# Kernel tuning notes

Measured on AMD Instinct MI355X. Metric: run time of the kernel, lower is better.

Reference implementation:

```python
import jax, jax.numpy as jnp
import numpy as np

EMA_BETA = 0.9
NUM_HEADS = 16

def causal_prefix_ema(x, beta):
    # x: [b, t, d]; s_t = beta*s_{t-1} + (1-beta)*x_t, s_{-1}=0
    def step(s, xt):
        s = beta * s + (1.0 - beta) * xt
        return s, s
    s0 = jnp.zeros_like(x[:, 0, :])
    _, ys = jax.lax.scan(step, s0, jnp.swapaxes(x, 0, 1))  # [t, b, d]
    return jnp.swapaxes(ys, 0, 1)

def setup_inputs() -> dict:
    key = jax.random.key(0)
    ks = jax.random.split(key, 9)
    b, t, d = 2, 1024, 2048
    sc = lambda fan_in: 1.0 / np.sqrt(fan_in)
    return {
        "x": jax.random.normal(ks[0], (b, t, d), jnp.float32),
        "l3_memory": jax.random.normal(ks[1], (b, 1, d), jnp.float32),
        "wq": jax.random.normal(ks[2], (d, d), jnp.float32) * sc(d),
        "wk": jax.random.normal(ks[3], (d, d), jnp.float32) * sc(d),
        "wv": jax.random.normal(ks[4], (d, d), jnp.float32) * sc(d),
        "wo": jax.random.normal(ks[5], (d, d), jnp.float32) * sc(d),
        "rw1": jax.random.normal(ks[6], (d // 2, d), jnp.float32) * sc(d),
        "rb1": jnp.zeros((d // 2,), jnp.float32),
        "rw2": jax.random.normal(ks[7], (3, d // 2), jnp.float32) * sc(d // 2),
        "rb2": jnp.zeros((3,), jnp.float32),
    }

def reference(x, l3_memory, wq, wk, wv, wo, rw1, rb1, rw2, rb2):
    b, t, d = x.shape
    h = NUM_HEADS
    dh = d // h
    scale = 1.0 / np.sqrt(dh)

    q = x @ wq.T                                   # [b,t,d]
    l1 = x
    l2 = causal_prefix_ema(x, EMA_BETA)            # [b,t,d]
    l3 = jnp.broadcast_to(l3_memory, (b, t, d))    # repeat retrieval memory to length t

    # router: MLP(Q) -> softmax over 3 levels
    hdn = jax.nn.silu(q @ rw1.T + rb1)
    lam = jax.nn.softmax(hdn @ rw2.T + rb2, axis=-1)  # [b,t,3]

    fused = lam[..., 0:1] * l1 + lam[..., 1:2] * l2 + lam[..., 2:3] * l3

    def heads(y):
        return jnp.swapaxes(y.reshape(b, t, h, dh), 1, 2)  # [b,h,t,dh]

    qh = heads(q)
    kh = heads(fused @ wk.T)
    vh = heads(fused @ wv.T)

    scores = jnp.einsum("bhqd,bhkd->bhqk", qh, kh) * scale
    causal = jnp.tril(jnp.ones((t, t), bool))
    scores = jnp.where(causal, scores, jnp.finfo(scores.dtype).min)
    attn = jax.nn.softmax(scores, axis=-1)
    out = jnp.einsum("bhqk,bhkd->bhqd", attn, vh)

    out = jnp.swapaxes(out, 1, 2).reshape(b, t, d) @ wo.T
    return (out, kh, vh, lam)
```

## Files before the change

kernel.cpp:

```cpp
#include <hip/hip_runtime.h>
#include <hip/hip_bf16.h>
#include <math.h>

#define B_  2
#define T_  1024
#define D_  2048
#define H_  16
#define DH_ 128
#define M_  2048
#define DR_ 1024
#define CH_  16
#define NCH_ 64

typedef __attribute__((ext_vector_type(8))) short short8;
typedef __attribute__((ext_vector_type(4))) short sh4;
typedef __attribute__((ext_vector_type(4))) float f32x4;

__device__ __forceinline__ void gld16(const __hip_bfloat16* g, __hip_bfloat16* l) {
  __builtin_amdgcn_global_load_lds(
      (const __attribute__((address_space(1))) unsigned int*)g,
      (__attribute__((address_space(3))) unsigned int*)l, 16, 0, 0);
}

template<int BM, int CMODE, bool SILU>
__global__ __launch_bounds__(256)
void gemm_mfma(const __hip_bfloat16* __restrict__ A,
               const __hip_bfloat16* __restrict__ Bm,
               const float* __restrict__ bias,
               float* __restrict__ C, __hip_bfloat16* __restrict__ Cb,
               float* __restrict__ C2, __hip_bfloat16* __restrict__ Cb2,
               int M, int N, int K)
{
  constexpr int NI = BM / 32;
  constexpr int AC = BM / 64;
  __shared__ __hip_bfloat16 As[2][2][BM * 32];
  __shared__ __hip_bfloat16 Bs[2][2][128 * 32];
  const int tid  = threadIdx.x;
  const int wave = tid >> 6;
  const int lane = tid & 63;
  const int m0 = blockIdx.y * BM;
  const int n0 = blockIdx.x * 128;
  const int wm = (wave >> 1) * (BM / 2);
  const int wn = (wave & 1) * 64;

  const int srow = lane >> 2;
  const int scol = (lane & 3) * 8;
  const __hip_bfloat16* Ag = A  + (size_t)(m0 + wave * (BM / 4) + srow) * K + scol;
  const __hip_bfloat16* Bg = Bm + (size_t)(n0 + wave * 32 + srow) * K + scol;

  const int fr = lane & 15;
  const int fk = (lane >> 4) * 8;

  f32x4 acc[NI][4];
  #pragma unroll
  for (int i = 0; i < NI; ++i)
    #pragma unroll
    for (int j = 0; j < 4; ++j) acc[i][j] = (f32x4)0.f;

  auto stage = [&](int bf, int k0) {
    #pragma unroll
    for (int h = 0; h < 2; ++h) {
      #pragma unroll
      for (int c = 0; c < AC; ++c)
        gld16(Ag + k0 + h * 32 + (size_t)(c * 16) * K,
              &As[bf][h][(wave * (BM / 4) + c * 16) * 32]);
      #pragma unroll
      for (int c = 0; c < 2; ++c)
        gld16(Bg + k0 + h * 32 + (size_t)(c * 16) * K,
              &Bs[bf][h][(wave * 32 + c * 16) * 32]);
    }
  };

  stage(0, 0);
  __syncthreads();
  int cur = 0;
  for (int k0 = 0; k0 < K; k0 += 64) {
    if (k0 + 64 < K) stage(cur ^ 1, k0 + 64);
    #pragma unroll
    for (int h = 0; h < 2; ++h) {
      short8 af[NI], bfr[4];
      #pragma unroll
      for (int i = 0; i < NI; ++i)
        af[i]  = *(const short8*)&As[cur][h][(wm + i * 16 + fr) * 32 + fk];
      #pragma unroll
      for (int j = 0; j < 4; ++j)
        bfr[j] = *(const short8*)&Bs[cur][h][(wn + j * 16 + fr) * 32 + fk];
      #pragma unroll
      for (int i = 0; i < NI; ++i)
        #pragma unroll
        for (int j = 0; j < 4; ++j)
          acc[i][j] = __builtin_amdgcn_mfma_f32_16x16x32_bf16(af[i], bfr[j], acc[i][j], 0, 0, 0);
    }
    __syncthreads();
    cur ^= 1;
  }

  #pragma unroll
  for (int i = 0; i < NI; ++i) {
    #pragma unroll
    for (int j = 0; j < 4; ++j) {
      const int row0 = m0 + wm + i * 16 + (lane >> 4) * 4;
      const int col  = n0 + wn + j * 16 + (lane & 15);
      float vr[4];
      #pragma unroll
      for (int r = 0; r < 4; ++r) {
        float v = acc[i][j][r];
        if (bias) v += bias[col];
        if (SILU) v = v / (1.f + __expf(-v));
        vr[r] = v;
      }
      if (CMODE == 0) {
        #pragma unroll
        for (int r = 0; r < 4; ++r) C[(size_t)(row0 + r) * N + col] = vr[r];
      } else if (CMODE == 1) {
        #pragma unroll
        for (int r = 0; r < 4; ++r) Cb[(size_t)(row0 + r) * N + col] = __float2bfloat16(vr[r]);
      } else {
        const int bb = row0 >> 10, t0v = row0 & 1023;
        if (col < D_) {
          const int hh = col >> 7, dd = col & 127;
          #pragma unroll
          for (int r = 0; r < 4; ++r) {
            const size_t idx = (((size_t)(bb * H_ + hh)) * T_ + t0v + r) * DH_ + dd;
            C[idx] = vr[r];
            Cb[idx] = __float2bfloat16(vr[r]);
          }
        } else {
          const int c2 = col - D_;
          const int hh = c2 >> 7, dd = c2 & 127;
          #pragma unroll
          for (int r = 0; r < 4; ++r)
            C2[(((size_t)(bb * H_ + hh)) * T_ + t0v + r) * DH_ + dd] = vr[r];
          __hip_bfloat16 tmp[4];
          #pragma unroll
          for (int r = 0; r < 4; ++r) tmp[r] = __float2bfloat16(vr[r]);
          *(sh4*)(Cb2 + (((size_t)(bb * H_ + hh)) * DH_ + dd) * T_ + t0v) = *(const sh4*)tmp;
        }
      }
    }
  }
}

__global__ __launch_bounds__(256)
void prep_scan(const float* __restrict__ x, __hip_bfloat16* __restrict__ xb,
               float* __restrict__ l2)
{
  const int b  = blockIdx.z;
  const int t0 = blockIdx.y * CH_;
  const int d  = blockIdx.x * 1024 + threadIdx.x * 4;
  const float* xp = x  + (size_t)b * T_ * D_ + d;
  float*       lp = l2 + (size_t)b * T_ * D_ + d;
  __hip_bfloat16* xo = xb + (size_t)b * T_ * D_ + d;
  float4 s = make_float4(0.f, 0.f, 0.f, 0.f);
  #pragma unroll 4
  for (int t = t0; t < t0 + CH_; ++t) {
    float4 v = *(const float4*)(xp + (size_t)t * D_);
    __hip_bfloat16 tmp[4] = {__float2bfloat16(v.x), __float2bfloat16(v.y),
                             __float2bfloat16(v.z), __float2bfloat16(v.w)};
    *(sh4*)(xo + (size_t)t * D_) = *(const sh4*)tmp;
    s.x = 0.9f * s.x + 0.1f * v.x;
    s.y = 0.9f * s.y + 0.1f * v.y;
    s.z = 0.9f * s.z + 0.1f * v.z;
    s.w = 0.9f * s.w + 0.1f * v.w;
    *(float4*)(lp + (size_t)t * D_) = s;
  }
}

__global__ __launch_bounds__(256)
void cvt5(const float* __restrict__ s0, const float* __restrict__ s1,
          const float* __restrict__ s2, const float* __restrict__ s3,
          const float* __restrict__ s4,
          __hip_bfloat16* d0, __hip_bfloat16* d1, __hip_bfloat16* d2,
          __hip_bfloat16* d3, __hip_bfloat16* d4,
          int n0, int n1, int n2, int n3, int n4)
{
  const float* s; __hip_bfloat16* d; int n;
  switch (blockIdx.y) {
    case 0: s = s0; d = d0; n = n0; break;
    case 1: s = s1; d = d1; n = n1; break;
    case 2: s = s2; d = d2; n = n2; break;
    case 3: s = s3; d = d3; n = n3; break;
    default: s = s4; d = d4; n = n4; break;
  }
  const int i = (blockIdx.x * 256 + threadIdx.x) * 8;
  if (i < n) {
    float4 a = *(const float4*)(s + i);
    float4 b = *(const float4*)(s + i + 4);
    __hip_bfloat16 t[8] = {__float2bfloat16(a.x), __float2bfloat16(a.y),
                           __float2bfloat16(a.z), __float2bfloat16(a.w),
                           __float2bfloat16(b.x), __float2bfloat16(b.y),
                           __float2bfloat16(b.z), __float2bfloat16(b.w)};
    *(short8*)(d + i) = *(const short8*)t;
  }
}

__global__ __launch_bounds__(64)
void ema_carry(const float* __restrict__ l2loc, float* __restrict__ carry)
{
  const int i = blockIdx.x * 64 + threadIdx.x;
  const int b = i >> 11, d = i & 2047;
  const float A = 0.18530201888518416f;
  float c = 0.f;
  carry[((size_t)b * NCH_ + 0) * D_ + d] = 0.f;
  for (int ch = 1; ch < NCH_; ++ch) {
    const float lf = l2loc[((size_t)b * T_ + ch * CH_ - 1) * D_ + d];
    c = lf + A * c;
    carry[((size_t)b * NCH_ + ch) * D_ + d] = c;
  }
}

__global__ __launch_bounds__(256)
void router_kernel(const float* __restrict__ hdn, const float* __restrict__ rw2,
                   const float* __restrict__ rb2, float* __restrict__ lam)
{
  const int lane = threadIdx.x & 63;
  const int w    = threadIdx.x >> 6;
  const int m    = blockIdx.x * 4 + w;
  const float* hp = hdn + (size_t)m * DR_;
  float s0 = 0.f, s1 = 0.f, s2 = 0.f;
  for (int k = lane * 4; k < DR_; k += 256) {
    float4 h4 = *(const float4*)(hp + k);
    float4 w0 = *(const float4*)(rw2 + k);
    float4 w1 = *(const float4*)(rw2 + DR_ + k);
    float4 w2 = *(const float4*)(rw2 + 2 * DR_ + k);
    s0 += h4.x * w0.x + h4.y * w0.y + h4.z * w0.z + h4.w * w0.w;
    s1 += h4.x * w1.x + h4.y * w1.y + h4.z * w1.z + h4.w * w1.w;
    s2 += h4.x * w2.x + h4.y * w2.y + h4.z * w2.z + h4.w * w2.w;
  }
  #pragma unroll
  for (int off = 32; off > 0; off >>= 1) {
    s0 += __shfl_down(s0, off);
    s1 += __shfl_down(s1, off);
    s2 += __shfl_down(s2, off);
  }
  if (lane == 0) {
    s0 += rb2[0]; s1 += rb2[1]; s2 += rb2[2];
    float mx = fmaxf(s0, fmaxf(s1, s2));
    float e0 = __expf(s0 - mx), e1 = __expf(s1 - mx), e2 = __expf(s2 - mx);
    float inv = 1.f / (e0 + e1 + e2);
    lam[(size_t)m * 3 + 0] = e0 * inv;
    lam[(size_t)m * 3 + 1] = e1 * inv;
    lam[(size_t)m * 3 + 2] = e2 * inv;
  }
}

__global__ __launch_bounds__(256)
void fuse_bf16(const float* __restrict__ x, const float* __restrict__ l2,
               const float* __restrict__ l3m, const float* __restrict__ lam,
               const float* __restrict__ carry, __hip_bfloat16* __restrict__ fb)
{
  const int i8 = blockIdx.x * 256 + threadIdx.x;
  const int m  = i8 >> 8;
  const int c  = (i8 & 255) << 3;
  const int b  = m >> 10;
  const int t  = m & 1023;
  const int ch = t >> 4, off = t & 15;
  const float p = __expf((float)(off + 1) * -0.105360515657f);
  const float w0 = lam[m * 3 + 0], w1 = lam[m * 3 + 1], w2 = lam[m * 3 + 2];
  const float* xp = x   + (size_t)m * D_ + c;
  const float* ep = l2  + (size_t)m * D_ + c;
  const float* gp = l3m + (size_t)b * D_ + c;
  const float* cp = carry + ((size_t)b * NCH_ + ch) * D_ + c;
  __hip_bfloat16 tmp[8];
  #pragma unroll
  for (int q = 0; q < 2; ++q) {
    float4 xv = *(const float4*)(xp + q * 4);
    float4 ev = *(const float4*)(ep + q * 4);
    float4 gv = *(const float4*)(gp + q * 4);
    float4 cv = *(const float4*)(cp + q * 4);
    tmp[q * 4 + 0] = __float2bfloat16(w0 * xv.x + w1 * (ev.x + p * cv.x) + w2 * gv.x);
    tmp[q * 4 + 1] = __float2bfloat16(w0 * xv.y + w1 * (ev.y + p * cv.y) + w2 * gv.y);
    tmp[q * 4 + 2] = __float2bfloat16(w0 * xv.z + w1 * (ev.z + p * cv.z) + w2 * gv.z);
    tmp[q * 4 + 3] = __float2bfloat16(w0 * xv.w + w1 * (ev.w + p * cv.w) + w2 * gv.w);
  }
  *(short8*)(fb + (size_t)m * D_ + c) = *(const short8*)tmp;
}

__global__ __launch_bounds__(256)
void flash_mfma(const __hip_bfloat16* __restrict__ qg,
                const __hip_bfloat16* __restrict__ kg,
                const __hip_bfloat16* __restrict__ vg,
                __hip_bfloat16* __restrict__ og)
{
  __shared__ __hip_bfloat16 Ks[64 * 136];
  __shared__ __hip_bfloat16 Vt[128 * 72];
  __shared__ __hip_bfloat16 Ps[64 * 72];
  const int tid  = threadIdx.x;
  const int wave = tid >> 6, lane = tid & 63;
  const int L    = blockIdx.x;
  const int halfg = L >> 8, idx = L & 255;
  const int bh = (idx >> 4) | (halfg << 4);
  const int qt = halfg ? (15 - (idx & 15)) : (idx & 15);
  const int b = bh >> 4, h = bh & 15;
  const int q0 = qt * 64;
  const int lo = lane & 15, hi = lane >> 4;

  short8 aq[4];
  {
    const __hip_bfloat16* qsrc = qg + (size_t)(b * T_ + q0 + wave * 16 + lo) * D_ + h * DH_;
    #pragma unroll
    for (int kk = 0; kk < 4; ++kk)
      aq[kk] = *(const short8*)(qsrc + kk * 32 + hi * 8);
  }

  f32x4 oacc[8];
  #pragma unroll
  for (int i = 0; i < 8; ++i) oacc[i] = (f32x4)0.f;
  float mrow[4] = {-INFINITY, -INFINITY, -INFINITY, -INFINITY};
  float lrow[4] = {0.f, 0.f, 0.f, 0.f};

  const __hip_bfloat16* kbp = kg + (size_t)bh * T_ * DH_;
  const __hip_bfloat16* vbp = vg + (size_t)bh * DH_ * T_;
  const float scale = 0.08838834764831845f;

  short8 kreg[4], vreg[4];
  auto load_tile = [&](int k0) {
    #pragma unroll
    for (int i = 0; i < 4; ++i) {
      const int ci = tid + 256 * i;
      const int r = ci >> 4, j = ci & 15;
      kreg[i] = *(const short8*)(kbp + (size_t)(k0 + r) * DH_ + j * 8);
      const int dd = ci >> 3, j2 = ci & 7;
      vreg[i] = *(const short8*)(vbp + (size_t)dd * T_ + k0 + j2 * 8);
    }
  };

  load_tile(0);
  for (int kt = 0; kt <= qt; ++kt) {
    #pragma unroll
    for (int i = 0; i < 4; ++i) {
      const int ci = tid + 256 * i;
      const int r = ci >> 4, j = ci & 15;
      *(short8*)&Ks[r * 136 + j * 8] = kreg[i];
      const int dd = ci >> 3, j2 = ci & 7;
      *(short8*)&Vt[dd * 72 + j2 * 8] = vreg[i];
    }
    __syncthreads();
    if (kt < qt) load_tile((kt + 1) * 64);

    f32x4 sc[4];
    __builtin_amdgcn_s_setprio(1);
    #pragma unroll
    for (int nt = 0; nt < 4; ++nt) {
      sc[nt] = (f32x4)0.f;
      #pragma unroll
      for (int kk = 0; kk < 4; ++kk) {
        short8 bk = *(const short8*)&Ks[(nt * 16 + lo) * 136 + kk * 32 + hi * 8];
        sc[nt] = __builtin_amdgcn_mfma_f32_16x16x32_bf16(aq[kk], bk, sc[nt], 0, 0, 0);
      }
    }
    __builtin_amdgcn_s_setprio(0);
    #pragma unroll
    for (int nt = 0; nt < 4; ++nt)
      #pragma unroll
      for (int r = 0; r < 4; ++r) sc[nt][r] *= scale;
    if (kt == qt) {
      const int qrow = q0 + wave * 16 + hi * 4;
      #pragma unroll
      for (int nt = 0; nt < 4; ++nt) {
        const int key = qt * 64 + nt * 16 + lo;
        #pragma unroll
        for (int r = 0; r < 4; ++r)
          if (key > qrow + r) sc[nt][r] = -1e30f;
      }
    }
    float alpha[4];
    #pragma unroll
    for (int r = 0; r < 4; ++r) {
      float mx = fmaxf(fmaxf(sc[0][r], sc[1][r]), fmaxf(sc[2][r], sc[3][r]));
      mx = fmaxf(mx, __shfl_xor(mx, 1));
      mx = fmaxf(mx, __shfl_xor(mx, 2));
      mx = fmaxf(mx, __shfl_xor(mx, 4));
      mx = fmaxf(mx, __shfl_xor(mx, 8));
      const float nm = fmaxf(mrow[r], mx);
      alpha[r] = __expf(mrow[r] - nm);
      mrow[r] = nm;
      float ls = 0.f;
      #pragma unroll
      for (int nt = 0; nt < 4; ++nt) {
        float p = __expf(sc[nt][r] - nm);
        sc[nt][r] = p;
        ls += p;
      }
      ls += __shfl_xor(ls, 1);
      ls += __shfl_xor(ls, 2);
      ls += __shfl_xor(ls, 4);
      ls += __shfl_xor(ls, 8);
      lrow[r] = lrow[r] * alpha[r] + ls;
    }
    #pragma unroll
    for (int nt = 0; nt < 4; ++nt)
      #pragma unroll
      for (int r = 0; r < 4; ++r)
        Ps[(wave * 16 + hi * 4 + r) * 72 + nt * 16 + lo] = __float2bfloat16(sc[nt][r]);
    #pragma unroll
    for (int n2 = 0; n2 < 8; ++n2)
      #pragma unroll
      for (int r = 0; r < 4; ++r) oacc[n2][r] *= alpha[r];
    short8 ap[2];
    #pragma unroll
    for (int k2 = 0; k2 < 2; ++k2)
      ap[k2] = *(const short8*)&Ps[(wave * 16 + lo) * 72 + k2 * 32 + hi * 8];
    __builtin_amdgcn_s_setprio(1);
    #pragma unroll
    for (int n2 = 0; n2 < 8; ++n2) {
      #pragma unroll
      for (int k2 = 0; k2 < 2; ++k2) {
        short8 bv = *(const short8*)&Vt[(n2 * 16 + lo) * 72 + k2 * 32 + hi * 8];
        oacc[n2] = __builtin_amdgcn_mfma_f32_16x16x32_bf16(ap[k2], bv, oacc[n2], 0, 0, 0);
      }
    }
    __builtin_amdgcn_s_setprio(0);
    __syncthreads();
  }

  float inv[4];
  #pragma unroll
  for (int r = 0; r < 4; ++r) inv[r] = 1.f / lrow[r];
  __hip_bfloat16* od = og + (size_t)(b * T_ + q0 + wave * 16 + hi * 4) * D_ + h * DH_;
  #pragma unroll
  for (int n2 = 0; n2 < 8; ++n2)
    #pragma unroll
    for (int r = 0; r < 4; ++r)
      od[(size_t)r * D_ + n2 * 16 + lo] = __float2bfloat16(oacc[n2][r] * inv[r]);
}

extern "C" void kernel_launch(void* const* d_in, const int* in_sizes, int n_in,
                              void* d_out, int out_size, void* d_ws, size_t ws_size,
                              hipStream_t stream)
{
  const float* x   = (const float*)d_in[0];
  const float* l3m = (const float*)d_in[1];
  const float* wq  = (const float*)d_in[2];
  const float* wk  = (const float*)d_in[3];
  const float* wv  = (const float*)d_in[4];
  const float* wo  = (const float*)d_in[5];
  const float* rw1 = (const float*)d_in[6];
  const float* rb1 = (const float*)d_in[7];
  const float* rw2 = (const float*)d_in[8];
  const float* rb2 = (const float*)d_in[9];

  float* out = (float*)d_out;
  float* kh  = out + 4194304;
  float* vh  = out + 8388608;
  float* lam = out + 12582912;

  char* wsb = (char*)d_ws;
  float*          l2_f32 = (float*)(wsb);
  float*          hdn    = (float*)(wsb + (16u << 20));
  __hip_bfloat16* wkb    = (__hip_bfloat16*)(wsb + (24u << 20));
  __hip_bfloat16* wvb    = (__hip_bfloat16*)(wsb + (32u << 20));
  __hip_bfloat16* wob    = (__hip_bfloat16*)(wsb + (40u << 20));
  __hip_bfloat16* fusedb = (__hip_bfloat16*)(wsb + (48u << 20));
  __hip_bfloat16* attnb  = (__hip_bfloat16*)(wsb + (56u << 20));
  __hip_bfloat16* khb    = (__hip_bfloat16*)(wsb + (64u << 20));
  __hip_bfloat16* vtb    = (__hip_bfloat16*)(wsb + (72u << 20));
  float*          carry  = (float*)attnb;
  __hip_bfloat16* wqb  = (__hip_bfloat16*)kh;
  __hip_bfloat16* rw1b = (__hip_bfloat16*)kh + 4194304;
  __hip_bfloat16* xb   = (__hip_bfloat16*)vh;
  __hip_bfloat16* qb   = (__hip_bfloat16*)out;

  dim3 blk(256);

  prep_scan<<<dim3(2, NCH_, 2), blk, 0, stream>>>(x, xb, l2_f32);
  cvt5<<<dim3(2048, 5), blk, 0, stream>>>(wq, wk, wv, wo, rw1,
                                          wqb, wkb, wvb, wob, rw1b,
                                          D_ * D_, D_ * D_, D_ * D_, D_ * D_, DR_ * D_);
  ema_carry<<<dim3(64), dim3(64), 0, stream>>>(l2_f32, carry);
  gemm_mfma<64, 1, false><<<dim3(16, 32), blk, 0, stream>>>(xb, wqb, nullptr, nullptr, qb, nullptr, nullptr, M_, D_, D_);
  gemm_mfma<64, 0, true><<<dim3(8, 32), blk, 0, stream>>>(qb, rw1b, rb1, hdn, nullptr, nullptr, nullptr, M_, DR_, D_);
  router_kernel<<<dim3(512), blk, 0, stream>>>(hdn, rw2, rb2, lam);
  fuse_bf16<<<dim3(2048), blk, 0, stream>>>(x, l2_f32, l3m, lam, carry, fusedb);
  gemm_mfma<128, 4, false><<<dim3(32, 16), blk, 0, stream>>>(fusedb, wkb, nullptr, kh, khb, vh, vtb, M_, 2 * D_, D_);
  flash_mfma<<<dim3(512), blk, 0, stream>>>(qb, khb, vtb, attnb);
  gemm_mfma<64, 0, false><<<dim3(16, 32), blk, 0, stream>>>(attnb, wob, nullptr, out, nullptr, nullptr, nullptr, M_, D_, D_);
}
```

Before: 349.3 us.

## Fuse prep kernels, parallelize EMA carry scan, merge router with fuse, double-buffer flash

Merges the x prep/EMA scan and weight conversion into one launch, and has each chunk write its final EMA state to a small buffer. The serial 64-thread carry loop becomes a wave-level parallel prefix scan. The router softmax is merged with the fused-input build so lambda stays in shared memory. Flash attention gets double-buffered K/V shared memory so the next tile's LDS write overlaps compute and one barrier per tile is removed. Together these cut launches and serial latency, at the cost of more LDS per flash block, which may lower occupancy.

```diff
diff --git a/kernel.cpp b/kernel.cpp
--- a/kernel.cpp
+++ b/kernel.cpp
@@ -142,45 +142,49 @@
 }
 
 __global__ __launch_bounds__(256)
-void prep_scan(const float* __restrict__ x, __hip_bfloat16* __restrict__ xb,
-               float* __restrict__ l2)
-{
-  const int b  = blockIdx.z;
-  const int t0 = blockIdx.y * CH_;
-  const int d  = blockIdx.x * 1024 + threadIdx.x * 4;
-  const float* xp = x  + (size_t)b * T_ * D_ + d;
-  float*       lp = l2 + (size_t)b * T_ * D_ + d;
-  __hip_bfloat16* xo = xb + (size_t)b * T_ * D_ + d;
-  float4 s = make_float4(0.f, 0.f, 0.f, 0.f);
-  #pragma unroll 4
-  for (int t = t0; t < t0 + CH_; ++t) {
-    float4 v = *(const float4*)(xp + (size_t)t * D_);
-    __hip_bfloat16 tmp[4] = {__float2bfloat16(v.x), __float2bfloat16(v.y),
-                             __float2bfloat16(v.z), __float2bfloat16(v.w)};
-    *(sh4*)(xo + (size_t)t * D_) = *(const sh4*)tmp;
-    s.x = 0.9f * s.x + 0.1f * v.x;
-    s.y = 0.9f * s.y + 0.1f * v.y;
-    s.z = 0.9f * s.z + 0.1f * v.z;
-    s.w = 0.9f * s.w + 0.1f * v.w;
-    *(float4*)(lp + (size_t)t * D_) = s;
-  }
-}
-
-__global__ __launch_bounds__(256)
-void cvt5(const float* __restrict__ s0, const float* __restrict__ s1,
-          const float* __restrict__ s2, const float* __restrict__ s3,
-          const float* __restrict__ s4,
-          __hip_bfloat16* d0, __hip_bfloat16* d1, __hip_bfloat16* d2,
-          __hip_bfloat16* d3, __hip_bfloat16* d4,
-          int n0, int n1, int n2, int n3, int n4)
-{
+void prep_all(const float* __restrict__ x, __hip_bfloat16* __restrict__ xb,
+              float* __restrict__ l2, float* __restrict__ lf,
+              const float* __restrict__ s1, const float* __restrict__ s2,
+              const float* __restrict__ s3, const float* __restrict__ s4,
+              const float* __restrict__ s5,
+              __hip_bfloat16* d1, __hip_bfloat16* d2, __hip_bfloat16* d3,
+              __hip_bfloat16* d4, __hip_bfloat16* d5,
+              int n1, int n2, int n3, int n4, int n5)
+{
+  if (blockIdx.y == 0) {
+    const int bid = blockIdx.x;
+    if (bid >= 256) return;
+    const int dblk = bid & 1;
+    const int ch   = (bid >> 1) & 63;
+    const int b    = bid >> 7;
+    const int t0 = ch * CH_;
+    const int d  = dblk * 1024 + threadIdx.x * 4;
+    const float* xp = x  + (size_t)b * T_ * D_ + d;
+    float*       lp = l2 + (size_t)b * T_ * D_ + d;
+    __hip_bfloat16* xo = xb + (size_t)b * T_ * D_ + d;
+    float4 s = make_float4(0.f, 0.f, 0.f, 0.f);
+    #pragma unroll 4
+    for (int t = t0; t < t0 + CH_; ++t) {
+      float4 v = *(const float4*)(xp + (size_t)t * D_);
+      __hip_bfloat16 tmp[4] = {__float2bfloat16(v.x), __float2bfloat16(v.y),
+                               __float2bfloat16(v.z), __float2bfloat16(v.w)};
+      *(sh4*)(xo + (size_t)t * D_) = *(const sh4*)tmp;
+      s.x = 0.9f * s.x + 0.1f * v.x;
+      s.y = 0.9f * s.y + 0.1f * v.y;
+      s.z = 0.9f * s.z + 0.1f * v.z;
+      s.w = 0.9f * s.w + 0.1f * v.w;
+      *(float4*)(lp + (size_t)t * D_) = s;
+    }
+    *(float4*)(lf + ((size_t)b * NCH_ + ch) * D_ + d) = s;
+    return;
+  }
   const float* s; __hip_bfloat16* d; int n;
   switch (blockIdx.y) {
-    case 0: s = s0; d = d0; n = n0; break;
     case 1: s = s1; d = d1; n = n1; break;
     case 2: s = s2; d = d2; n = n2; break;
     case 3: s = s3; d = d3; n = n3; break;
-    default: s = s4; d = d4; n = n4; break;
+    case 4: s = s4; d = d4; n = n4; break;
+    default: s = s5; d = d5; n = n5; break;
   }
   const int i = (blockIdx.x * 256 + threadIdx.x) * 8;
   if (i < n) {
@@ -194,31 +198,41 @@
   }
 }
 
-__global__ __launch_bounds__(64)
-void ema_carry(const float* __restrict__ l2loc, float* __restrict__ carry)
-{
-  const int i = blockIdx.x * 64 + threadIdx.x;
-  const int b = i >> 11, d = i & 2047;
-  const float A = 0.18530201888518416f;
-  float c = 0.f;
-  carry[((size_t)b * NCH_ + 0) * D_ + d] = 0.f;
-  for (int ch = 1; ch < NCH_; ++ch) {
-    const float lf = l2loc[((size_t)b * T_ + ch * CH_ - 1) * D_ + d];
-    c = lf + A * c;
-    carry[((size_t)b * NCH_ + ch) * D_ + d] = c;
-  }
-}
-
 __global__ __launch_bounds__(256)
-void router_kernel(const float* __restrict__ hdn, const float* __restrict__ rw2,
-                   const float* __restrict__ rb2, float* __restrict__ lam)
-{
+void ema_carry_scan(const float* __restrict__ lf, float* __restrict__ carry)
+{
+  const int wid  = (blockIdx.x * 256 + threadIdx.x) >> 6;
   const int lane = threadIdx.x & 63;
-  const int w    = threadIdx.x >> 6;
-  const int m    = blockIdx.x * 4 + w;
+  const int b = wid >> 11, d = wid & 2047;
+  float S = lf[((size_t)b * NCH_ + lane) * D_ + d];
+  float p = 0.18530201888518416f;
+  #pragma unroll
+  for (int off = 1; off < 64; off <<= 1) {
+    float Su = __shfl_up(S, off);
+    float pu = __shfl_up(p, off);
+    if (lane >= off) { S = S + p * Su; p = p * pu; }
+  }
+  float c = __shfl_up(S, 1);
+  if (lane == 0) c = 0.f;
+  carry[((size_t)b * NCH_ + lane) * D_ + d] = c;
+}
+
+__global__ __launch_bounds__(256)
+void fuse_router(const float* __restrict__ x, const float* __restrict__ l2,
+                 const float* __restrict__ l3m, const float* __restrict__ hdn,
+                 const float* __restrict__ rw2, const float* __restrict__ rb2,
+                 const float* __restrict__ carry, float* __restrict__ lam,
+                 __hip_bfloat16* __restrict__ fb)
+{
+  __shared__ float lamS[8][3];
+  const int tid = threadIdx.x;
+  const int g = tid >> 5, l32 = tid & 31;
+  const int m = blockIdx.x * 8 + g;
   const float* hp = hdn + (size_t)m * DR_;
   float s0 = 0.f, s1 = 0.f, s2 = 0.f;
-  for (int k = lane * 4; k < DR_; k += 256) {
+  #pragma unroll
+  for (int it = 0; it < 8; ++it) {
+    const int k = l32 * 4 + it * 128;
     float4 h4 = *(const float4*)(hp + k);
     float4 w0 = *(const float4*)(rw2 + k);
     float4 w1 = *(const float4*)(rw2 + DR_ + k);
@@ -228,12 +242,12 @@
     s2 += h4.x * w2.x + h4.y * w2.y + h4.z * w2.z + h4.w * w2.w;
   }
   #pragma unroll
-  for (int off = 32; off > 0; off >>= 1) {
-    s0 += __shfl_down(s0, off);
-    s1 += __shfl_down(s1, off);
-    s2 += __shfl_down(s2, off);
-  }
-  if (lane == 0) {
+  for (int off = 16; off > 0; off >>= 1) {
+    s0 += __shfl_xor(s0, off);
+    s1 += __shfl_xor(s1, off);
+    s2 += __shfl_xor(s2, off);
+  }
+  if (l32 == 0) {
     s0 += rb2[0]; s1 += rb2[1]; s2 += rb2[2];
     float mx = fmaxf(s0, fmaxf(s1, s2));
     float e0 = __expf(s0 - mx), e1 = __expf(s1 - mx), e2 = __expf(s2 - mx);
@@ -241,39 +255,36 @@
     lam[(size_t)m * 3 + 0] = e0 * inv;
     lam[(size_t)m * 3 + 1] = e1 * inv;
     lam[(size_t)m * 3 + 2] = e2 * inv;
-  }
-}
-
-__global__ __launch_bounds__(256)
-void fuse_bf16(const float* __restrict__ x, const float* __restrict__ l2,
-               const float* __restrict__ l3m, const float* __restrict__ lam,
-               const float* __restrict__ carry, __hip_bfloat16* __restrict__ fb)
-{
-  const int i8 = blockIdx.x * 256 + threadIdx.x;
-  const int m  = i8 >> 8;
-  const int c  = (i8 & 255) << 3;
-  const int b  = m >> 10;
-  const int t  = m & 1023;
-  const int ch = t >> 4, off = t & 15;
-  const float p = __expf((float)(off + 1) * -0.105360515657f);
-  const float w0 = lam[m * 3 + 0], w1 = lam[m * 3 + 1], w2 = lam[m * 3 + 2];
-  const float* xp = x   + (size_t)m * D_ + c;
-  const float* ep = l2  + (size_t)m * D_ + c;
-  const float* gp = l3m + (size_t)b * D_ + c;
-  const float* cp = carry + ((size_t)b * NCH_ + ch) * D_ + c;
-  __hip_bfloat16 tmp[8];
-  #pragma unroll
-  for (int q = 0; q < 2; ++q) {
-    float4 xv = *(const float4*)(xp + q * 4);
-    float4 ev = *(const float4*)(ep + q * 4);
-    float4 gv = *(const float4*)(gp + q * 4);
-    float4 cv = *(const float4*)(cp + q * 4);
-    tmp[q * 4 + 0] = __float2bfloat16(w0 * xv.x + w1 * (ev.x + p * cv.x) + w2 * gv.x);
-    tmp[q * 4 + 1] = __float2bfloat16(w0 * xv.y + w1 * (ev.y + p * cv.y) + w2 * gv.y);
-    tmp[q * 4 + 2] = __float2bfloat16(w0 * xv.z + w1 * (ev.z + p * cv.z) + w2 * gv.z);
-    tmp[q * 4 + 3] = __float2bfloat16(w0 * xv.w + w1 * (ev.w + p * cv.w) + w2 * gv.w);
-  }
-  *(short8*)(fb + (size_t)m * D_ + c) = *(const short8*)tmp;
+    lamS[g][0] = e0 * inv; lamS[g][1] = e1 * inv; lamS[g][2] = e2 * inv;
+  }
+  __syncthreads();
+
+  const int c = tid * 8;
+  #pragma unroll
+  for (int r = 0; r < 8; ++r) {
+    const int mm = blockIdx.x * 8 + r;
+    const int bb = mm >> 10, tt = mm & 1023;
+    const int ch = tt >> 4, off = tt & 15;
+    const float pw = __expf((float)(off + 1) * -0.105360515657f);
+    const float u0 = lamS[r][0], u1 = lamS[r][1], u2 = lamS[r][2];
+    const float* xp = x   + (size_t)mm * D_ + c;
+    const float* ep = l2  + (size_t)mm * D_ + c;
+    const float* gp = l3m + (size_t)bb * D_ + c;
+    const float* cp = carry + ((size_t)bb * NCH_ + ch) * D_ + c;
+    __hip_bfloat16 tmp[8];
+    #pragma unroll
+    for (int q = 0; q < 2; ++q) {
+      float4 xv = *(const float4*)(xp + q * 4);
+      float4 ev = *(const float4*)(ep + q * 4);
+      float4 gv = *(const float4*)(gp + q * 4);
+      float4 cv = *(const float4*)(cp + q * 4);
+      tmp[q * 4 + 0] = __float2bfloat16(u0 * xv.x + u1 * (ev.x + pw * cv.x) + u2 * gv.x);
+      tmp[q * 4 + 1] = __float2bfloat16(u0 * xv.y + u1 * (ev.y + pw * cv.y) + u2 * gv.y);
+      tmp[q * 4 + 2] = __float2bfloat16(u0 * xv.z + u1 * (ev.z + pw * cv.z) + u2 * gv.z);
+      tmp[q * 4 + 3] = __float2bfloat16(u0 * xv.w + u1 * (ev.w + pw * cv.w) + u2 * gv.w);
+    }
+    *(short8*)(fb + (size_t)mm * D_ + c) = *(const short8*)tmp;
+  }
 }
 
 __global__ __launch_bounds__(256)
@@ -282,8 +293,8 @@
                 const __hip_bfloat16* __restrict__ vg,
                 __hip_bfloat16* __restrict__ og)
 {
-  __shared__ __hip_bfloat16 Ks[64 * 136];
-  __shared__ __hip_bfloat16 Vt[128 * 72];
+  __shared__ __hip_bfloat16 Ks[2][64 * 136];
+  __shared__ __hip_bfloat16 Vt[2][128 * 72];
   __shared__ __hip_bfloat16 Ps[64 * 72];
   const int tid  = threadIdx.x;
   const int wave = tid >> 6, lane = tid & 63;
@@ -324,20 +335,24 @@
       vreg[i] = *(const short8*)(vbp + (size_t)dd * T_ + k0 + j2 * 8);
     }
   };
-
-  load_tile(0);
-  for (int kt = 0; kt <= qt; ++kt) {
+  auto write_lds = [&](int bf) {
     #pragma unroll
     for (int i = 0; i < 4; ++i) {
       const int ci = tid + 256 * i;
       const int r = ci >> 4, j = ci & 15;
-      *(short8*)&Ks[r * 136 + j * 8] = kreg[i];
+      *(short8*)&Ks[bf][r * 136 + j * 8] = kreg[i];
       const int dd = ci >> 3, j2 = ci & 7;
-      *(short8*)&Vt[dd * 72 + j2 * 8] = vreg[i];
-    }
-    __syncthreads();
-    if (kt < qt) load_tile((kt + 1) * 64);
-
+      *(short8*)&Vt[bf][dd * 72 + j2 * 8] = vreg[i];
+    }
+  };
+
+  load_tile(0);
+  write_lds(0);
+  if (qt > 0) load_tile(64);
+  __syncthreads();
+
+  for (int kt = 0; kt <= qt; ++kt) {
+    const int cur = kt & 1;
     f32x4 sc[4];
     __builtin_amdgcn_s_setprio(1);
     #pragma unroll
@@ -345,7 +360,7 @@
       sc[nt] = (f32x4)0.f;
       #pragma unroll
       for (int kk = 0; kk < 4; ++kk) {
-        short8 bk = *(const short8*)&Ks[(nt * 16 + lo) * 136 + kk * 32 + hi * 8];
+        short8 bk = *(const short8*)&Ks[cur][(nt * 16 + lo) * 136 + kk * 32 + hi * 8];
         sc[nt] = __builtin_amdgcn_mfma_f32_16x16x32_bf16(aq[kk], bk, sc[nt], 0, 0, 0);
       }
     }
@@ -406,11 +421,15 @@
     for (int n2 = 0; n2 < 8; ++n2) {
       #pragma unroll
       for (int k2 = 0; k2 < 2; ++k2) {
-        short8 bv = *(const short8*)&Vt[(n2 * 16 + lo) * 72 + k2 * 32 + hi * 8];
+        short8 bv = *(const short8*)&Vt[cur][(n2 * 16 + lo) * 72 + k2 * 32 + hi * 8];
         oacc[n2] = __builtin_amdgcn_mfma_f32_16x16x32_bf16(ap[k2], bv, oacc[n2], 0, 0, 0);
       }
     }
     __builtin_amdgcn_s_setprio(0);
+    if (kt < qt) {
+      write_lds(cur ^ 1);
+      if (kt + 1 < qt) load_tile((kt + 2) * 64);
+    }
     __syncthreads();
   }
 
@@ -456,6 +475,7 @@
   __hip_bfloat16* khb    = (__hip_bfloat16*)(wsb + (64u << 20));
   __hip_bfloat16* vtb    = (__hip_bfloat16*)(wsb + (72u << 20));
   float*          carry  = (float*)attnb;
+  float*          lf     = (float*)(wsb + (57u << 20));
   __hip_bfloat16* wqb  = (__hip_bfloat16*)kh;
   __hip_bfloat16* rw1b = (__hip_bfloat16*)kh + 4194304;
   __hip_bfloat16* xb   = (__hip_bfloat16*)vh;
@@ -463,15 +483,14 @@
 
   dim3 blk(256);
 
-  prep_scan<<<dim3(2, NCH_, 2), blk, 0, stream>>>(x, xb, l2_f32);
-  cvt5<<<dim3(2048, 5), blk, 0, stream>>>(wq, wk, wv, wo, rw1,
-                                          wqb, wkb, wvb, wob, rw1b,
-                                          D_ * D_, D_ * D_, D_ * D_, D_ * D_, DR_ * D_);
-  ema_carry<<<dim3(64), dim3(64), 0, stream>>>(l2_f32, carry);
+  prep_all<<<dim3(2048, 6), blk, 0, stream>>>(x, xb, l2_f32, lf,
+                                              wq, wk, wv, wo, rw1,
+                                              wqb, wkb, wvb, wob, rw1b,
+                                              D_ * D_, D_ * D_, D_ * D_, D_ * D_, DR_ * D_);
+  ema_carry_scan<<<dim3(1024), blk, 0, stream>>>(lf, carry);
   gemm_mfma<64, 1, false><<<dim3(16, 32), blk, 0, stream>>>(xb, wqb, nullptr, nullptr, qb, nullptr, nullptr, M_, D_, D_);
   gemm_mfma<64, 0, true><<<dim3(8, 32), blk, 0, stream>>>(qb, rw1b, rb1, hdn, nullptr, nullptr, nullptr, M_, DR_, D_);
-  router_kernel<<<dim3(512), blk, 0, stream>>>(hdn, rw2, rb2, lam);
-  fuse_bf16<<<dim3(2048), blk, 0, stream>>>(x, l2_f32, l3m, lam, carry, fusedb);
+  fuse_router<<<dim3(256), blk, 0, stream>>>(x, l2_f32, l3m, hdn, rw2, rb2, carry, lam, fusedb);
   gemm_mfma<128, 4, false><<<dim3(32, 16), blk, 0, stream>>>(fusedb, wkb, nullptr, kh, khb, vh, vtb, M_, 2 * D_, D_);
   flash_mfma<<<dim3(512), blk, 0, stream>>>(qb, khb, vtb, attnb);
   gemm_mfma<64, 0, false><<<dim3(16, 32), blk, 0, stream>>>(attnb, wob, nullptr, out, nullptr, nullptr, nullptr, M_, D_, D_);
```

After: 343.7 us. No clear change (-1.6%).
